# Kernel tuning notes

Measured on AMD Instinct MI355X. Metric: run time of the kernel, lower is better.

Reference implementation:

```python
import jax, jax.numpy as jnp
import numpy as np

NUM_STUDENTS = 50000
NUM_PROBLEMS = 10000
EMBED_DIM = 64
NNZ = 3200000


def _spmm(rows, cols, vals, x, num_out):
    # out[r] = sum_{edges e with rows[e]==r} vals[e] * x[cols[e]]
    msgs = vals[:, None] * x[cols]  # [nnz, d]
    return jax.ops.segment_sum(msgs, rows, num_segments=num_out)


def setup_inputs() -> dict:
    key = jax.random.key(0)
    ks = jax.random.split(key, 8)
    return {
        "student_embeds": jax.random.normal(ks[0], (NUM_STUDENTS, EMBED_DIM), jnp.float32),
        "problem_embeds": jax.random.normal(ks[1], (NUM_PROBLEMS, EMBED_DIM), jnp.float32),
        "a_rows": jax.random.randint(ks[2], (NNZ,), 0, NUM_STUDENTS, jnp.int32),
        "a_cols": jax.random.randint(ks[3], (NNZ,), 0, NUM_PROBLEMS, jnp.int32),
        "a_vals": jax.random.uniform(ks[4], (NNZ,), jnp.float32),
        "ia_rows": jax.random.randint(ks[5], (NNZ,), 0, NUM_STUDENTS, jnp.int32),
        "ia_cols": jax.random.randint(ks[6], (NNZ,), 0, NUM_PROBLEMS, jnp.int32),
        "ia_vals": jax.random.uniform(ks[7], (NNZ,), jnp.float32),
    }


def reference(student_embeds, problem_embeds, a_rows, a_cols, a_vals,
              ia_rows, ia_cols, ia_vals):
    num_students = student_embeds.shape[0]
    num_problems = problem_embeds.shape[0]
    # a_matrix @ problem_embeds
    student_embeds_c = _spmm(a_rows, a_cols, a_vals, problem_embeds, num_students)
    # a_matrix.T @ student_embeds (swap roles of rows/cols)
    problem_embeds_c = _spmm(a_cols, a_rows, a_vals, student_embeds, num_problems)
    student_embeds_ic = _spmm(ia_rows, ia_cols, ia_vals, problem_embeds, num_students)
    problem_embeds_ic = _spmm(ia_cols, ia_rows, ia_vals, student_embeds, num_problems)
    return (student_embeds_c, student_embeds_ic, problem_embeds_c, problem_embeds_ic)
```

## Files before the change

kernel.cpp:

```cpp
#include <hip/hip_runtime.h>
#include <hip/hip_bf16.h>

#define NBMAX 256
#define TILE  4096
#define KPT   16
#define BINSMAX 512
#define SLP   520

__device__ __forceinline__ int seg8(unsigned r, unsigned mult8) {
    return (int)__umulhi(r, mult8);
}

__global__ __launch_bounds__(256) void hist_all(
        const int* __restrict__ k0, const int* __restrict__ k1,
        const int* __restrict__ k2, const int* __restrict__ k3,
        int* __restrict__ gcnt4, int nnz, int rsh_s, int rsh_p) {
    __shared__ int h[NBMAX];
    int dir = blockIdx.x & 3;
    const int* key = (dir == 0) ? k0 : (dir == 1) ? k1 : (dir == 2) ? k2 : k3;
    int rsh = (dir & 1) ? rsh_p : rsh_s;
    h[threadIdx.x] = 0;
    __syncthreads();
    int ch = blockIdx.x >> 2, nch = gridDim.x >> 2;
    int nnz4 = nnz >> 2;
    for (int i = ch * 256 + threadIdx.x; i < nnz4; i += nch * 256) {
        int4 k4 = ((const int4*)key)[i];
        atomicAdd(&h[k4.x >> rsh], 1);
        atomicAdd(&h[k4.y >> rsh], 1);
        atomicAdd(&h[k4.z >> rsh], 1);
        atomicAdd(&h[k4.w >> rsh], 1);
    }
    if (ch == 0) {
        for (int i = (nnz4 << 2) + threadIdx.x; i < nnz; i += 256)
            atomicAdd(&h[key[i] >> rsh], 1);
    }
    __syncthreads();
    int v = h[threadIdx.x];
    if (v) atomicAdd(&gcnt4[dir * NBMAX + threadIdx.x], v);
}

__global__ __launch_bounds__(256) void scan_all(
        const int* __restrict__ gcnt4, int* __restrict__ boffs4,
        int* __restrict__ bcur4, int nb_s, int nb_p, int nnz,
        int* __restrict__ offsE, int* __restrict__ offsO, int NS, int NP8) {
    __shared__ int tmp[NBMAX];
    int dir = blockIdx.x, tid = threadIdx.x;
    int nb = (dir & 1) ? nb_p : nb_s;
    int v = (tid < nb) ? gcnt4[dir * NBMAX + tid] : 0;
    tmp[tid] = v;
    __syncthreads();
    for (int off = 1; off < NBMAX; off <<= 1) {
        int t = (tid >= off) ? tmp[tid - off] : 0;
        __syncthreads();
        tmp[tid] += t;
        __syncthreads();
    }
    if (tid < nb) {
        int e = tmp[tid] - v;
        boffs4[dir * (NBMAX + 1) + tid] = e;
        bcur4[dir * NBMAX + tid] = e;
    }
    if (tid == 0) boffs4[dir * (NBMAX + 1) + nb] = nnz;
    if (dir == 0 && tid == 0) { offsE[NS] = nnz; offsO[NP8] = nnz; }
}

__global__ __launch_bounds__(256) void staged_scatter(
        const int* __restrict__ key, const int* __restrict__ other,
        const float* __restrict__ vals, int* __restrict__ cursor,
        uint2* __restrict__ edges, int nnz, int rsh) {
    __shared__ int lhist[NBMAX], lofs[NBMAX], lbase[NBMAX];
    __shared__ uint2 stage[TILE];
    __shared__ int   sslot[TILE];
    int tid = threadIdx.x;
    int lmask = (1 << rsh) - 1;
    int ntiles = (nnz + TILE - 1) / TILE;
    for (int tile = blockIdx.x; tile < ntiles; tile += gridDim.x) {
        int tbeg = tile * TILE;
        int n = nnz - tbeg; if (n > TILE) n = TILE;
        lhist[tid] = 0;
        __syncthreads();
        int myb[KPT], myr[KPT]; unsigned myo[KPT]; float myv[KPT];
        #pragma unroll
        for (int g = 0; g < 4; ++g) {
            int s = g * 1024 + tid * 4;
            if (s + 4 <= n) {
                int i = tbeg + s;
                int4   k4 = *(const int4*)(key + i);
                int4   o4 = *(const int4*)(other + i);
                float4 v4 = *(const float4*)(vals + i);
                int   kk[4] = {k4.x, k4.y, k4.z, k4.w};
                int   oo[4] = {o4.x, o4.y, o4.z, o4.w};
                float vv[4] = {v4.x, v4.y, v4.z, v4.w};
                #pragma unroll
                for (int k = 0; k < 4; ++k) {
                    int m = g * 4 + k;
                    myb[m] = kk[k] >> rsh;
                    myo[m] = (unsigned)oo[k] | ((unsigned)(kk[k] & lmask) << 16);
                    myv[m] = vv[k];
                    myr[m] = atomicAdd(&lhist[myb[m]], 1);
                }
            } else {
                #pragma unroll
                for (int k = 0; k < 4; ++k) {
                    int m = g * 4 + k;
                    int s2 = s + k;
                    if (s2 < n) {
                        int i = tbeg + s2;
                        int ky = key[i];
                        myb[m] = ky >> rsh;
                        myo[m] = (unsigned)other[i] | ((unsigned)(ky & lmask) << 16);
                        myv[m] = vals[i];
                        myr[m] = atomicAdd(&lhist[myb[m]], 1);
                    } else myb[m] = -1;
                }
            }
        }
        __syncthreads();
        int h = lhist[tid];
        lofs[tid] = h;
        __syncthreads();
        for (int off = 1; off < NBMAX; off <<= 1) {
            int t = (tid >= off) ? lofs[tid - off] : 0;
            __syncthreads();
            lofs[tid] += t;
            __syncthreads();
        }
        lofs[tid] -= h;
        if (h > 0) lbase[tid] = atomicAdd(&cursor[tid], h);
        __syncthreads();
        #pragma unroll
        for (int k = 0; k < KPT; ++k) {
            if (myb[k] >= 0) {
                int ls = lofs[myb[k]] + myr[k];
                stage[ls] = make_uint2(myo[k], __float_as_uint(myv[k]));
                sslot[ls] = lbase[myb[k]] + myr[k];
            }
        }
        __syncthreads();
        #pragma unroll
        for (int k = 0; k < KPT; ++k) {
            int s = k * 256 + tid;
            if (s < n) edges[sslot[s]] = stage[s];
        }
        __syncthreads();
    }
}

__global__ __launch_bounds__(512) void row_scatter2(
        const uint2* __restrict__ e1, uint2* __restrict__ e2,
        const int* __restrict__ boffs, int* __restrict__ offs,
        int odd, int nb, int rsh, int nrows, unsigned mult8) {
    __shared__ int cnt[8 * SLP];
    __shared__ int tot[512];
    __shared__ int lcur[BINSMAX];
    int tid = threadIdx.x;
    int g = blockIdx.x;
    int x = g & 7;
    int sk = (g >> 3) & 7;
    int bi = g >> 6;
    int b = x + 8 * bi;
    if (b >= nb) return;
    int bins = odd ? (8 << rsh) : (1 << rsh);
    int beg = boffs[b], end = boffs[b + 1];
    int len = end - beg;
    for (int i = tid; i < 8 * SLP; i += 512) cnt[i] = 0;
    __syncthreads();
    int psh = 0;
    {
        int per = (len + 7) >> 3;
        while ((1 << psh) < per) psh++;
    }
    if (len > 0) {
        for (int i = beg + tid; i < end; i += 512) {
            uint2 e = e1[i];
            int lrow = (int)(e.x >> 16);
            int bin = odd ? (lrow * 8 + seg8(e.x & 0xFFFFu, mult8)) : lrow;
            int sl = (i - beg) >> psh;
            atomicAdd(&cnt[sl * SLP + bin], 1);
        }
    }
    __syncthreads();
    int own = 0;
    if (tid < bins) {
        #pragma unroll
        for (int j = 0; j < 8; ++j) own += cnt[j * SLP + tid];
    }
    tot[tid] = (tid < bins) ? own : 0;
    __syncthreads();
    for (int off = 1; off < 512; off <<= 1) {
        int t = (tid >= off) ? tot[tid - off] : 0;
        __syncthreads();
        tot[tid] += t;
        __syncthreads();
    }
    if (tid < bins) {
        int fineoff = tot[tid] - own;
        int basej = 0;
        for (int j = 0; j < sk; ++j) basej += cnt[j * SLP + tid];
        lcur[tid] = beg + fineoff + basej;
        if (sk == 0) {
            if (!odd) {
                int row = (b << rsh) + tid;
                if (row < nrows) offs[row] = beg + fineoff;
            } else {
                int row = (b << rsh) + (tid >> 3);
                if (row < nrows) offs[(row << 3) + (tid & 7)] = beg + fineoff;
            }
        }
    }
    __syncthreads();
    int lo = beg + (sk << psh);
    int hi = lo + (1 << psh); if (hi > end) hi = end;
    for (int i = lo + tid; i < hi; i += 512) {
        uint2 e = e1[i];
        int lrow = (int)(e.x >> 16);
        int bin = odd ? (lrow * 8 + seg8(e.x & 0xFFFFu, mult8)) : lrow;
        int slot = atomicAdd(&lcur[bin], 1);
        e2[slot] = make_uint2(e.x & 0xFFFFu, e.y);
    }
}

__device__ __forceinline__ void chunk_accum(
        float4& acc, uint2 e, int n, const float* __restrict__ xq, int q) {
    int   c0 = __shfl((int)e.x, q);
    float v0 = __uint_as_float(__shfl((int)e.y, q));
    int   c1 = __shfl((int)e.x, 4 + q);
    float v1 = __uint_as_float(__shfl((int)e.y, 4 + q));
    float4 x0 = *(const float4*)(xq + (((size_t)c0) << 6));
    float4 x1 = *(const float4*)(xq + (((size_t)c1) << 6));
    for (int j = 8; j < n; j += 8) {
        int   nc0 = __shfl((int)e.x, j + q);
        float nv0 = __uint_as_float(__shfl((int)e.y, j + q));
        int   nc1 = __shfl((int)e.x, j + 4 + q);
        float nv1 = __uint_as_float(__shfl((int)e.y, j + 4 + q));
        float4 nx0 = *(const float4*)(xq + (((size_t)nc0) << 6));
        float4 nx1 = *(const float4*)(xq + (((size_t)nc1) << 6));
        acc.x += v0 * x0.x; acc.y += v0 * x0.y;
        acc.z += v0 * x0.z; acc.w += v0 * x0.w;
        acc.x += v1 * x1.x; acc.y += v1 * x1.y;
        acc.z += v1 * x1.z; acc.w += v1 * x1.w;
        v0 = nv0; v1 = nv1; x0 = nx0; x1 = nx1;
    }
    acc.x += v0 * x0.x; acc.y += v0 * x0.y;
    acc.z += v0 * x0.z; acc.w += v0 * x0.w;
    acc.x += v1 * x1.x; acc.y += v1 * x1.y;
    acc.z += v1 * x1.z; acc.w += v1 * x1.w;
}

__device__ __forceinline__ float4 gather_pre(
        uint2 e0, int beg, int end, const uint2* __restrict__ edges,
        const float* __restrict__ xq, int q, int lane) {
    float4 acc = make_float4(0.f, 0.f, 0.f, 0.f);
    int n0 = end - beg; if (n0 > 64) n0 = 64;
    chunk_accum(acc, e0, n0, xq, q);
    for (int base = beg + 64; base < end; base += 64) {
        int n = end - base; if (n > 64) n = 64;
        uint2 e = make_uint2(0u, 0u);
        if (lane < n) e = edges[base + lane];
        chunk_accum(acc, e, n, xq, q);
    }
    acc.x += __shfl_xor(acc.x, 16); acc.y += __shfl_xor(acc.y, 16);
    acc.z += __shfl_xor(acc.z, 16); acc.w += __shfl_xor(acc.w, 16);
    acc.x += __shfl_xor(acc.x, 32); acc.y += __shfl_xor(acc.y, 32);
    acc.z += __shfl_xor(acc.z, 32); acc.w += __shfl_xor(acc.w, 32);
    return acc;
}

__global__ __launch_bounds__(256) void row_gather(
        const int* __restrict__ offs, const uint2* __restrict__ edges,
        const float* __restrict__ x, float* __restrict__ out, int nrows) {
    int wave = threadIdx.x >> 6, lane = threadIdx.x & 63;
    int q = lane >> 4, l16 = lane & 15;
    const float* xq = x + (l16 << 2);
    int rA = blockIdx.x * 8 + wave * 2;
    if (rA >= nrows) return;
    int rB = rA + 1;
    int begA = offs[rA], endA = offs[rA + 1];
    int begB = 0, endB = 0;
    if (rB < nrows) { begB = offs[rB]; endB = offs[rB + 1]; }
    int nA = endA - begA; if (nA > 64) nA = 64;
    int nB = endB - begB; if (nB > 64) nB = 64;
    uint2 eA = make_uint2(0u, 0u), eB = make_uint2(0u, 0u);
    if (lane < nA) eA = edges[begA + lane];
    if (lane < nB) eB = edges[begB + lane];
    float4 accA = gather_pre(eA, begA, endA, edges, xq, q, lane);
    if ((lane >> 4) == 0)
        *(float4*)(out + (((size_t)rA) << 6) + (l16 << 2)) = accA;
    if (rB < nrows) {
        float4 accB = gather_pre(eB, begB, endB, edges, xq, q, lane);
        if ((lane >> 4) == 0)
            *(float4*)(out + (((size_t)rB) << 6) + (l16 << 2)) = accB;
    }
}

__global__ __launch_bounds__(256) void xcd_gather(
        const int* __restrict__ offs, const uint2* __restrict__ edges,
        const float* __restrict__ x, float* __restrict__ partial, int NP) {
    int g = blockIdx.x;
    int slot = g & 7;
    int t = g >> 3;
    int wave = threadIdx.x >> 6, lane = threadIdx.x & 63;
    int q = lane >> 4, l16 = lane & 15;
    const float* xq = x + (l16 << 2);
    int rA = t * 8 + wave * 2;
    if (rA >= NP) return;
    int rB = rA + 1;
    int binA = rA * 8 + slot;
    int begA = offs[binA], endA = offs[binA + 1];
    int begB = 0, endB = 0;
    if (rB < NP) { int binB = rB * 8 + slot; begB = offs[binB]; endB = offs[binB + 1]; }
    int nA = endA - begA; if (nA > 64) nA = 64;
    int nB = endB - begB; if (nB > 64) nB = 64;
    uint2 eA = make_uint2(0u, 0u), eB = make_uint2(0u, 0u);
    if (lane < nA) eA = edges[begA + lane];
    if (lane < nB) eB = edges[begB + lane];
    float4 accA = gather_pre(eA, begA, endA, edges, xq, q, lane);
    if ((lane >> 4) == 0)
        *(float4*)(partial + (size_t)slot * NP * 64 + (((size_t)rA) << 6) + (l16 << 2)) = accA;
    if (rB < NP) {
        float4 accB = gather_pre(eB, begB, endB, edges, xq, q, lane);
        if ((lane >> 4) == 0)
            *(float4*)(partial + (size_t)slot * NP * 64 + (((size_t)rB) << 6) + (l16 << 2)) = accB;
    }
}

__global__ __launch_bounds__(256) void reduce8(
        const float* __restrict__ partial, float* __restrict__ out, int n4) {
    int i = blockIdx.x * 256 + threadIdx.x;
    if (i < n4) {
        const float4* p = (const float4*)partial;
        float4 s = make_float4(0.f, 0.f, 0.f, 0.f);
        #pragma unroll
        for (int xx = 0; xx < 8; ++xx) {
            float4 v = p[(size_t)xx * n4 + i];
            s.x += v.x; s.y += v.y; s.z += v.z; s.w += v.w;
        }
        ((float4*)out)[i] = s;
    }
}

__global__ void spmm_scatter_kernel(const int* __restrict__ rows, const int* __restrict__ cols,
                                    const float* __restrict__ vals,
                                    const float* __restrict__ s_emb, const float* __restrict__ p_emb,
                                    float* __restrict__ out_s, float* __restrict__ out_p, int nnz) {
    long long t = (long long)blockIdx.x * blockDim.x + threadIdx.x;
    int e = (int)(t >> 6);
    int d = (int)(t & 63);
    if (e >= nnz) return;
    int r = rows[e];
    int c = cols[e];
    float v = vals[e];
    atomicAdd(&out_s[(size_t)r * 64 + d], v * p_emb[(size_t)c * 64 + d]);
    atomicAdd(&out_p[(size_t)c * 64 + d], v * s_emb[(size_t)r * 64 + d]);
}

extern "C" void kernel_launch(void* const* d_in, const int* in_sizes, int n_in,
                              void* d_out, int out_size, void* d_ws, size_t ws_size,
                              hipStream_t stream) {
    const float* s_emb   = (const float*)d_in[0];
    const float* p_emb   = (const float*)d_in[1];
    const int*   a_rows  = (const int*)d_in[2];
    const int*   a_cols  = (const int*)d_in[3];
    const float* a_vals  = (const float*)d_in[4];
    const int*   ia_rows = (const int*)d_in[5];
    const int*   ia_cols = (const int*)d_in[6];
    const float* ia_vals = (const float*)d_in[7];

    const int NS  = in_sizes[0] / 64;
    const int NP  = in_sizes[1] / 64;
    const int nnz = in_sizes[2];
    const int NP8 = NP * 8;

    float* out = (float*)d_out;
    float* out_sc  = out;
    float* out_sic = out_sc  + (size_t)NS * 64;
    float* out_pc  = out_sic + (size_t)NS * 64;
    float* out_pic = out_pc  + (size_t)NP * 64;

    int rsh_s = 0; while ((((long long)NS + (1LL << rsh_s) - 1) >> rsh_s) > NBMAX) rsh_s++;
    int rsh_p = 0; while ((((long long)NP + (1LL << rsh_p) - 1) >> rsh_p) > NBMAX) rsh_p++;
    int nb_s = (NS + (1 << rsh_s) - 1) >> rsh_s;
    int nb_p = (NP + (1 << rsh_p) - 1) >> rsh_p;
    unsigned mult8 = (unsigned)((8ULL << 32) / (unsigned)NS);

    const size_t edges_bytes = (size_t)nnz * sizeof(uint2);
    const size_t offsE_bytes = (size_t)(NS + 1) * sizeof(int);
    const size_t offsO_bytes = (size_t)(NP8 + 1) * sizeof(int);
    const size_t need = 2 * edges_bytes + offsE_bytes + offsO_bytes
                      + (size_t)(4 * NBMAX + 4 * (NBMAX + 1) + 4 * NBMAX) * sizeof(int) + 256;
    const bool packable = (NS <= 0xFFFF) && (NP <= 0xFFFF) &&
                          ((1 << rsh_s) <= BINSMAX) && ((8 << rsh_p) <= BINSMAX) &&
                          (edges_bytes >= (size_t)NP8 * 64 * sizeof(float)) &&
                          ((NP * 64) % 4 == 0);

    if (ws_size < need || !packable) {
        hipMemsetAsync(d_out, 0, (size_t)out_size * sizeof(float), stream);
        const long long total = (long long)nnz * 64;
        const int grid = (int)((total + 255) / 256);
        spmm_scatter_kernel<<<grid, 256, 0, stream>>>(a_rows, a_cols, a_vals, s_emb, p_emb,
                                                      out_sc, out_pc, nnz);
        spmm_scatter_kernel<<<grid, 256, 0, stream>>>(ia_rows, ia_cols, ia_vals, s_emb, p_emb,
                                                      out_sic, out_pic, nnz);
        return;
    }

    char* w = (char*)d_ws;
    uint2* edges1 = (uint2*)w;  w += edges_bytes;
    uint2* edges2 = (uint2*)w;  w += edges_bytes;
    int*   offsE  = (int*)w;    w += offsE_bytes;
    int*   offsO  = (int*)w;    w += offsO_bytes;
    int*   gcnt4  = (int*)w;    w += 4 * NBMAX * sizeof(int);
    int*   boffs4 = (int*)w;    w += 4 * (NBMAX + 1) * sizeof(int);
    int*   bcur4  = (int*)w;
    float* partial = (float*)edges1;

    hipMemsetAsync(gcnt4, 0, 4 * NBMAX * sizeof(int), stream);
    hist_all<<<1024, 256, 0, stream>>>(a_rows, a_cols, ia_rows, ia_cols,
                                       gcnt4, nnz, rsh_s, rsh_p);
    scan_all<<<4, 256, 0, stream>>>(gcnt4, boffs4, bcur4, nb_s, nb_p, nnz,
                                    offsE, offsO, NS, NP8);

    const int ntiles = (nnz + TILE - 1) / TILE;
    const int grid_rs_s = 64 * ((nb_s + 7) / 8);
    const int grid_rs_p = 64 * ((nb_p + 7) / 8);

    struct Dir { const int* key; const int* other; const float* vals;
                 float* out; int odd; };
    Dir dirs[4] = {
        { a_rows,  a_cols,  a_vals,  out_sc,  0 },
        { a_cols,  a_rows,  a_vals,  out_pc,  1 },
        { ia_rows, ia_cols, ia_vals, out_sic, 0 },
        { ia_cols, ia_rows, ia_vals, out_pic, 1 },
    };
    for (int t = 0; t < 4; ++t) {
        const Dir& D = dirs[t];
        if (!D.odd) {
            staged_scatter<<<ntiles, 256, 0, stream>>>(D.key, D.other, D.vals,
                                                       bcur4 + t * NBMAX, edges1, nnz, rsh_s);
            row_scatter2<<<grid_rs_s, 512, 0, stream>>>(edges1, edges2,
                                                        boffs4 + t * (NBMAX + 1), offsE,
                                                        0, nb_s, rsh_s, NS, mult8);
            row_gather<<<(NS + 7) / 8, 256, 0, stream>>>(offsE, edges2, p_emb, D.out, NS);
        } else {
            staged_scatter<<<ntiles, 256, 0, stream>>>(D.key, D.other, D.vals,
                                                       bcur4 + t * NBMAX, edges1, nnz, rsh_p);
            row_scatter2<<<grid_rs_p, 512, 0, stream>>>(edges1, edges2,
                                                        boffs4 + t * (NBMAX + 1), offsO,
                                                        1, nb_p, rsh_p, NP, mult8);
            xcd_gather<<<8 * ((NP + 7) / 8), 256, 0, stream>>>(offsO, edges2,
                                                               s_emb, partial, NP);
            reduce8<<<(NP * 64 / 4 + 255) / 256, 256, 0, stream>>>(partial, D.out, NP * 64 / 4);
        }
    }
}
```

Before: 615.2 us.

## Replace split-bucket row scatter with single-block-per-bucket counting sort

Each bucket's local counting sort now runs in one 512-thread block instead of eight blocks that each recount the whole bucket into per-slice histograms. This removes the redundant histogram passes and the larger shared-memory footprint. The cost is far fewer blocks in flight and longer serial work per block.

```diff
diff --git a/kernel.cpp b/kernel.cpp
--- a/kernel.cpp
+++ b/kernel.cpp
@@ -5,7 +5,6 @@
 #define TILE  4096
 #define KPT   16
 #define BINSMAX 512
-#define SLP   520
 
 __device__ __forceinline__ int seg8(unsigned r, unsigned mult8) {
     return (int)__umulhi(r, mult8);
@@ -146,76 +145,52 @@
     }
 }
 
-__global__ __launch_bounds__(512) void row_scatter2(
+__global__ __launch_bounds__(512) void row_sort1(
         const uint2* __restrict__ e1, uint2* __restrict__ e2,
         const int* __restrict__ boffs, int* __restrict__ offs,
         int odd, int nb, int rsh, int nrows, unsigned mult8) {
-    __shared__ int cnt[8 * SLP];
+    __shared__ int cnt[BINSMAX];
     __shared__ int tot[512];
-    __shared__ int lcur[BINSMAX];
     int tid = threadIdx.x;
-    int g = blockIdx.x;
-    int x = g & 7;
-    int sk = (g >> 3) & 7;
-    int bi = g >> 6;
-    int b = x + 8 * bi;
+    int b = blockIdx.x;
     if (b >= nb) return;
     int bins = odd ? (8 << rsh) : (1 << rsh);
     int beg = boffs[b], end = boffs[b + 1];
-    int len = end - beg;
-    for (int i = tid; i < 8 * SLP; i += 512) cnt[i] = 0;
-    __syncthreads();
-    int psh = 0;
-    {
-        int per = (len + 7) >> 3;
-        while ((1 << psh) < per) psh++;
-    }
-    if (len > 0) {
-        for (int i = beg + tid; i < end; i += 512) {
-            uint2 e = e1[i];
-            int lrow = (int)(e.x >> 16);
-            int bin = odd ? (lrow * 8 + seg8(e.x & 0xFFFFu, mult8)) : lrow;
-            int sl = (i - beg) >> psh;
-            atomicAdd(&cnt[sl * SLP + bin], 1);
-        }
-    }
-    __syncthreads();
-    int own = 0;
-    if (tid < bins) {
-        #pragma unroll
-        for (int j = 0; j < 8; ++j) own += cnt[j * SLP + tid];
-    }
-    tot[tid] = (tid < bins) ? own : 0;
-    __syncthreads();
-    for (int off = 1; off < 512; off <<= 1) {
-        int t = (tid >= off) ? tot[tid - off] : 0;
-        __syncthreads();
-        tot[tid] += t;
-        __syncthreads();
-    }
-    if (tid < bins) {
-        int fineoff = tot[tid] - own;
-        int basej = 0;
-        for (int j = 0; j < sk; ++j) basej += cnt[j * SLP + tid];
-        lcur[tid] = beg + fineoff + basej;
-        if (sk == 0) {
-            if (!odd) {
-                int row = (b << rsh) + tid;
-                if (row < nrows) offs[row] = beg + fineoff;
-            } else {
-                int row = (b << rsh) + (tid >> 3);
-                if (row < nrows) offs[(row << 3) + (tid & 7)] = beg + fineoff;
-            }
-        }
-    }
-    __syncthreads();
-    int lo = beg + (sk << psh);
-    int hi = lo + (1 << psh); if (hi > end) hi = end;
-    for (int i = lo + tid; i < hi; i += 512) {
+    if (tid < bins) cnt[tid] = 0;
+    __syncthreads();
+    for (int i = beg + tid; i < end; i += 512) {
         uint2 e = e1[i];
         int lrow = (int)(e.x >> 16);
         int bin = odd ? (lrow * 8 + seg8(e.x & 0xFFFFu, mult8)) : lrow;
-        int slot = atomicAdd(&lcur[bin], 1);
+        atomicAdd(&cnt[bin], 1);
+    }
+    __syncthreads();
+    int own = (tid < bins) ? cnt[tid] : 0;
+    tot[tid] = own;
+    __syncthreads();
+    for (int off = 1; off < 512; off <<= 1) {
+        int t = (tid >= off) ? tot[tid - off] : 0;
+        __syncthreads();
+        tot[tid] += t;
+        __syncthreads();
+    }
+    if (tid < bins) {
+        int fineoff = tot[tid] - own;
+        cnt[tid] = beg + fineoff;
+        if (!odd) {
+            int row = (b << rsh) + tid;
+            if (row < nrows) offs[row] = beg + fineoff;
+        } else {
+            int row = (b << rsh) + (tid >> 3);
+            if (row < nrows) offs[(row << 3) + (tid & 7)] = beg + fineoff;
+        }
+    }
+    __syncthreads();
+    for (int i = beg + tid; i < end; i += 512) {
+        uint2 e = e1[i];
+        int lrow = (int)(e.x >> 16);
+        int bin = odd ? (lrow * 8 + seg8(e.x & 0xFFFFu, mult8)) : lrow;
+        int slot = atomicAdd(&cnt[bin], 1);
         e2[slot] = make_uint2(e.x & 0xFFFFu, e.y);
     }
 }
@@ -421,8 +396,6 @@
                                     offsE, offsO, NS, NP8);
 
     const int ntiles = (nnz + TILE - 1) / TILE;
-    const int grid_rs_s = 64 * ((nb_s + 7) / 8);
-    const int grid_rs_p = 64 * ((nb_p + 7) / 8);
 
     struct Dir { const int* key; const int* other; const float* vals;
                  float* out; int odd; };
@@ -437,16 +410,16 @@
         if (!D.odd) {
             staged_scatter<<<ntiles, 256, 0, stream>>>(D.key, D.other, D.vals,
                                                        bcur4 + t * NBMAX, edges1, nnz, rsh_s);
-            row_scatter2<<<grid_rs_s, 512, 0, stream>>>(edges1, edges2,
-                                                        boffs4 + t * (NBMAX + 1), offsE,
-                                                        0, nb_s, rsh_s, NS, mult8);
+            row_sort1<<<nb_s, 512, 0, stream>>>(edges1, edges2,
+                                                boffs4 + t * (NBMAX + 1), offsE,
+                                                0, nb_s, rsh_s, NS, mult8);
             row_gather<<<(NS + 7) / 8, 256, 0, stream>>>(offsE, edges2, p_emb, D.out, NS);
         } else {
             staged_scatter<<<ntiles, 256, 0, stream>>>(D.key, D.other, D.vals,
                                                        bcur4 + t * NBMAX, edges1, nnz, rsh_p);
-            row_scatter2<<<grid_rs_p, 512, 0, stream>>>(edges1, edges2,
-                                                        boffs4 + t * (NBMAX + 1), offsO,
-                                                        1, nb_p, rsh_p, NP, mult8);
+            row_sort1<<<nb_p, 512, 0, stream>>>(edges1, edges2,
+                                                boffs4 + t * (NBMAX + 1), offsO,
+                                                1, nb_p, rsh_p, NP, mult8);
             xcd_gather<<<8 * ((NP + 7) / 8), 256, 0, stream>>>(offsO, edges2,
                                                                s_emb, partial, NP);
             reduce8<<<(NP * 64 / 4 + 255) / 256, 256, 0, stream>>>(partial, D.out, NP * 64 / 4);
```

New measurement: 579.3 us. 5.8% less time.
